# Optimization experiments

Measured on AMD Instinct MI355X. Metric: run time of the kernel, lower is better.

The kernel has to match this reference:

```python
import jax, jax.numpy as jnp
import numpy as np

D_MODEL = 1024
D_STATE = 64
D_CONV = 4
HEADDIM = 64
EXPAND = 2
NGROUPS = 1
D_INNER = EXPAND * D_MODEL            # 2048
NHEADS = D_INNER // HEADDIM           # 32
CONV_DIM = D_INNER + 2 * NGROUPS * D_STATE
D_IN_PROJ = 2 * D_INNER + 2 * NGROUPS * D_STATE + NHEADS
FFN_DIM = 4096
B_SZ = 2
SEQ = 2048


def layernorm(x, w, b, eps=1e-5):
    m = jnp.mean(x, axis=-1, keepdims=True)
    v = jnp.var(x, axis=-1, keepdims=True)
    return (x - m) * jax.lax.rsqrt(v + eps) * w + b


def silu(x):
    return x * jax.nn.sigmoid(x)


def causal_dwconv(x, w, b):
    # x: [B, L, C], w: [C, K] depthwise, b: [C]; causal (left) padding
    xc = jnp.transpose(x, (0, 2, 1))                       # [B, C, L]
    xc = jnp.pad(xc, ((0, 0), (0, 0), (D_CONV - 1, 0)))
    k = w[:, None, :]                                      # [C, 1, K]
    y = jax.lax.conv_general_dilated(
        xc, k, window_strides=(1,), padding='VALID',
        dimension_numbers=('NCH', 'OIH', 'NCH'),
        feature_group_count=CONV_DIM)
    return jnp.transpose(y, (0, 2, 1)) + b                 # [B, L, C]


def mamba2(x, in_proj_w, conv_w, conv_b, dt_bias, A_log, D_param, norm_w, out_proj_w):
    Bsz, L, _ = x.shape
    zxbcdt = x @ in_proj_w.T                               # [B, L, D_IN_PROJ]
    z, xBC, dt = jnp.split(zxbcdt, [D_INNER, D_INNER + CONV_DIM], axis=-1)
    dt = jax.nn.softplus(dt + dt_bias)                     # [B, L, H]
    xBC = silu(causal_dwconv(xBC, conv_w, conv_b))
    xs, Bm, Cm = jnp.split(xBC, [D_INNER, D_INNER + NGROUPS * D_STATE], axis=-1)
    xs = xs.reshape(Bsz, L, NHEADS, HEADDIM)
    Bm = Bm.reshape(Bsz, L, NGROUPS, D_STATE)
    Cm = Cm.reshape(Bsz, L, NGROUPS, D_STATE)
    hpg = NHEADS // NGROUPS
    Bh = jnp.repeat(Bm, hpg, axis=2)                       # [B, L, H, N]
    Ch = jnp.repeat(Cm, hpg, axis=2)                       # [B, L, H, N]
    A = -jnp.exp(A_log)                                    # [H]
    dA = jnp.exp(dt * A)                                   # [B, L, H]

    # time-major for scan
    def step(h, inp):
        dA_t, dt_t, x_t, B_t, C_t = inp                    # [B,H], [B,H], [B,H,P], [B,H,N], [B,H,N]
        h = h * dA_t[:, :, None, None] + (dt_t[:, :, None, None] * x_t[..., None]) * B_t[:, :, None, :]
        y_t = jnp.einsum('bhpn,bhn->bhp', h, C_t)
        return h, y_t

    h0 = jnp.zeros((Bsz, NHEADS, HEADDIM, D_STATE), dtype=x.dtype)
    xs_tm = (jnp.moveaxis(dA, 1, 0), jnp.moveaxis(dt, 1, 0),
             jnp.moveaxis(xs, 1, 0), jnp.moveaxis(Bh, 1, 0), jnp.moveaxis(Ch, 1, 0))
    _, ys = jax.lax.scan(step, h0, xs_tm)                  # [L, B, H, P]
    y = jnp.moveaxis(ys, 0, 1) + D_param[None, None, :, None] * xs
    y = y.reshape(Bsz, L, D_INNER)
    # gated RMSNorm: RMSNorm(y * silu(z)) * weight
    y = y * silu(z)
    y = y * jax.lax.rsqrt(jnp.mean(jnp.square(y), axis=-1, keepdims=True) + 1e-5) * norm_w
    return y @ out_proj_w.T                                # [B, L, D_MODEL]


def setup_inputs() -> dict:
    key = jax.random.key(0)
    ks = jax.random.split(key, 12)
    s = 0.02
    inp = {
        'x': jax.random.normal(ks[0], (B_SZ, SEQ, D_MODEL), dtype=jnp.float32),
        'ln0_w': jnp.ones((D_MODEL,), jnp.float32), 'ln0_b': jnp.zeros((D_MODEL,), jnp.float32),
        'ln1_w': jnp.ones((D_MODEL,), jnp.float32), 'ln1_b': jnp.zeros((D_MODEL,), jnp.float32),
        'ln2_w': jnp.ones((D_MODEL,), jnp.float32), 'ln2_b': jnp.zeros((D_MODEL,), jnp.float32),
        'in_proj_w': jax.random.normal(ks[1], (D_IN_PROJ, D_MODEL), jnp.float32) * s,
        'conv_w': jax.random.normal(ks[2], (CONV_DIM, D_CONV), jnp.float32) * 0.2,
        'conv_b': jnp.zeros((CONV_DIM,), jnp.float32),
        'dt_bias': jax.random.uniform(ks[3], (NHEADS,), jnp.float32, -4.0, -1.0),
        'A_log': jnp.log(jnp.arange(1, NHEADS + 1, dtype=jnp.float32)),
        'D_param': jnp.ones((NHEADS,), jnp.float32),
        'norm_w': jnp.ones((D_INNER,), jnp.float32),
        'out_proj_w': jax.random.normal(ks[4], (D_MODEL, D_INNER), jnp.float32) * s,
        'ffn_w1': jax.random.normal(ks[5], (FFN_DIM, D_MODEL), jnp.float32) * s,
        'ffn_b1': jnp.zeros((FFN_DIM,), jnp.float32),
        'ffn_w2': jax.random.normal(ks[6], (D_MODEL, FFN_DIM), jnp.float32) * s,
        'ffn_b2': jnp.zeros((D_MODEL,), jnp.float32),
    }
    return inp


def reference(x, ln0_w, ln0_b, ln1_w, ln1_b, ln2_w, ln2_b, in_proj_w, conv_w, conv_b,
              dt_bias, A_log, D_param, norm_w, out_proj_w, ffn_w1, ffn_b1, ffn_w2, ffn_b2):
    x = layernorm(x, ln0_w, ln0_b)                                  # ln0 (layer_id==0)
    m = mamba2(layernorm(x, ln1_w, ln1_b), in_proj_w, conv_w, conv_b,
               dt_bias, A_log, D_param, norm_w, out_proj_w)
    x = x + m                                                        # dropout is identity in eval
    h = layernorm(x, ln2_w, ln2_b)
    h = jax.nn.gelu(h @ ffn_w1.T + ffn_b1, approximate=False) @ ffn_w2.T + ffn_b2
    return x + h
```

## Files before the change

### kernel.cpp

```cpp
#include <hip/hip_runtime.h>
#include <hip/hip_bf16.h>
#include <math.h>

typedef __hip_bfloat16 bf16;
typedef __bf16 bhalf;
typedef bhalf bhalf8 __attribute__((ext_vector_type(8)));
typedef float f32x4 __attribute__((ext_vector_type(4)));
typedef unsigned short u16;
typedef u16 u16x4 __attribute__((ext_vector_type(4)));
typedef u16 u16x8 __attribute__((ext_vector_type(8)));

#define D_MODEL   1024
#define D_STATE   64
#define HEADDIM   64
#define D_INNER   2048
#define NHEADS    32
#define CONV_DIM  2176
#define D_IN_PROJ 4256
#define FFN_DIM   4096
#define BSZ       2
#define SEQ       2048
#define NROWS     (BSZ*SEQ)
#define TC        64
#define NCH       (SEQ/TC)

#define AS1 __attribute__((address_space(1)))
#define AS3 __attribute__((address_space(3)))
__device__ __forceinline__ void load_lds16(const void* g, void* l) {
  __builtin_amdgcn_global_load_lds((AS1 void*)g, (AS3 void*)l, 16, 0, 0);
}

__device__ __forceinline__ float bf2f(u16 u) {
  return __uint_as_float(((unsigned)u) << 16);
}
__device__ __forceinline__ u16 f2bbits(float f) {
  bf16 h = __float2bfloat16(f);
  return *(u16*)&h;
}

#define NT 18
struct CvtArgs {
  const void* src[NT];
  void*       dst[NT];
  int ccum[NT + 1];
  int nel[NT];
};

__global__ __launch_bounds__(256)
void cvt_kernel(CvtArgs a, const unsigned short* __restrict__ x0,
                int* __restrict__ flagp)
{
  __shared__ int sbad;
  if (threadIdx.x == 0) sbad = 0;
  __syncthreads();
  {
    float v = bf2f(x0[threadIdx.x]);
    if (!(fabsf(v) <= 1e6f)) sbad = 1;
  }
  __syncthreads();
  const int isf32 = sbad;
  if (blockIdx.x == 0 && threadIdx.x == 0) *flagp = isf32;

  int c = blockIdx.x;
  int ti = 0;
  while (c >= a.ccum[ti + 1]) ti++;
  int j = (c - a.ccum[ti]) * 2048 + threadIdx.x * 8;
  if (j >= a.nel[ti]) return;
  if (isf32) {
    const float* s = (const float*)a.src[ti];
    f32x4 v0 = *(const f32x4*)(s + j);
    f32x4 v1 = *(const f32x4*)(s + j + 4);
    u16x8 o;
    #pragma unroll
    for (int k = 0; k < 4; k++) { o[k] = f2bbits(v0[k]); o[k + 4] = f2bbits(v1[k]); }
    *(u16x8*)((u16*)a.dst[ti] + j) = o;
  } else {
    *(u16x8*)((u16*)a.dst[ti] + j) = *(const u16x8*)((const u16*)a.src[ti] + j);
  }
}

template<int EPI>
__global__ __launch_bounds__(256, 2)
void gemm_bt(const bf16* __restrict__ A, const bf16* __restrict__ W,
             int M, int N, int K,
             bf16* __restrict__ outB,
             const bf16* __restrict__ bias)
{
  __shared__ __align__(16) bhalf sA[2][128 * 64];
  __shared__ __align__(16) bhalf sW[2][128 * 64];
  const int nbx   = gridDim.x;
  const int total = nbx * gridDim.y;
  const int lin   = blockIdx.y * nbx + blockIdx.x;
  const int chunk = total >> 3;
  const int swz   = ((total & 7) == 0) ? ((lin & 7) * chunk + (lin >> 3)) : lin;
  const int n0   = (swz % nbx) * 128;
  const int m0   = (swz / nbx) * 128;
  const int t    = threadIdx.x;
  const int w    = t >> 6;
  const int lane = t & 63;
  const int wm   = (w >> 1) * 64;
  const int wn   = (w & 1) * 64;
  const int lr   = lane & 15;
  const int lq   = lane >> 4;

  f32x4 acc[4][4];
  #pragma unroll
  for (int i = 0; i < 4; i++)
    #pragma unroll
    for (int j = 0; j < 4; j++)
      acc[i][j] = (f32x4){0.f, 0.f, 0.f, 0.f};

  auto stage = [&](int buf, int kk0) {
    #pragma unroll
    for (int j = 0; j < 4; j++) {
      int s  = t + 256 * j;
      int r  = s >> 3;
      int cs = (s & 7) ^ (r & 7);
      load_lds16(A + (size_t)(m0 + r) * K + kk0 + cs * 8, &sA[buf][s * 8]);
      int wr = n0 + r; wr = wr < N ? wr : N - 1;
      load_lds16(W + (size_t)wr * K + kk0 + cs * 8, &sW[buf][s * 8]);
    }
  };

  stage(0, 0);

  int cur = 0;
  for (int k0 = 0; k0 < K; k0 += 64) {
    const bool more = (k0 + 64 < K);
    if (more) stage(cur ^ 1, k0 + 64);
    if (more) asm volatile("s_waitcnt vmcnt(8)" ::: "memory");
    else      asm volatile("s_waitcnt vmcnt(0)" ::: "memory");
    __builtin_amdgcn_s_barrier();
    asm volatile("" ::: "memory");

    const bhalf* pA = sA[cur];
    const bhalf* pW = sW[cur];
    #pragma unroll
    for (int kk = 0; kk < 2; kk++) {
      bhalf8 af[4], bfr[4];
      #pragma unroll
      for (int i = 0; i < 4; i++) {
        int r = wm + i * 16 + lr;
        int c = (kk * 4 + lq) ^ (r & 7);
        af[i] = *(const bhalf8*)(pA + r * 64 + c * 8);
      }
      #pragma unroll
      for (int j = 0; j < 4; j++) {
        int r = wn + j * 16 + lr;
        int c = (kk * 4 + lq) ^ (r & 7);
        bfr[j] = *(const bhalf8*)(pW + r * 64 + c * 8);
      }
      #pragma unroll
      for (int i = 0; i < 4; i++)
        #pragma unroll
        for (int j = 0; j < 4; j++)
          acc[i][j] = __builtin_amdgcn_mfma_f32_16x16x32_bf16(af[i], bfr[j], acc[i][j], 0, 0, 0);
    }
    __builtin_amdgcn_s_barrier();
    asm volatile("" ::: "memory");
    cur ^= 1;
  }

  #pragma unroll
  for (int i = 0; i < 4; i++) {
    #pragma unroll
    for (int j = 0; j < 4; j++) {
      #pragma unroll
      for (int r = 0; r < 4; r++) {
        int m = m0 + wm + i * 16 + lq * 4 + r;
        int n = n0 + wn + j * 16 + lr;
        if (n < N) {
          float v = acc[i][j][r];
          size_t idx = (size_t)m * N + n;
          if (EPI == 0) {
            outB[idx] = __float2bfloat16(v);
          } else {
            v += __bfloat162float(bias[n]);
            outB[idx] = __float2bfloat16(0.5f * v * (1.0f + erff(v * 0.70710678118654752f)));
          }
        }
      }
    }
  }
}

template<int EPI>
__global__ __launch_bounds__(512, 2)
void gemm256_bt(const bf16* __restrict__ A, const bf16* __restrict__ W,
                int M, int N, int K,
                bf16* __restrict__ outB,
                const bf16* __restrict__ bias)
{
  __shared__ __align__(16) bhalf sA[2][256 * 64];
  __shared__ __align__(16) bhalf sW[2][256 * 64];
  const int nbx   = gridDim.x;
  const int total = nbx * gridDim.y;
  const int lin   = blockIdx.y * nbx + blockIdx.x;
  const int chunk = total >> 3;
  const int swz   = ((total & 7) == 0) ? ((lin & 7) * chunk + (lin >> 3)) : lin;
  const int n0   = (swz % nbx) * 256;
  const int m0   = (swz / nbx) * 256;
  const int t    = threadIdx.x;
  const int w    = t >> 6;
  const int lane = t & 63;
  const int wm   = (w >> 2) * 128;
  const int wn   = (w & 3) * 64;
  const int lr   = lane & 15;
  const int lq   = lane >> 4;

  f32x4 acc[8][4];
  #pragma unroll
  for (int i = 0; i < 8; i++)
    #pragma unroll
    for (int j = 0; j < 4; j++)
      acc[i][j] = (f32x4){0.f, 0.f, 0.f, 0.f};

  auto stage = [&](int buf, int kk0) {
    #pragma unroll
    for (int j = 0; j < 4; j++) {
      int s  = t + 512 * j;
      int r  = s >> 3;
      int cs = (s & 7) ^ (r & 7);
      load_lds16(A + (size_t)(m0 + r) * K + kk0 + cs * 8, &sA[buf][s * 8]);
    }
    #pragma unroll
    for (int j = 0; j < 4; j++) {
      int s  = t + 512 * j;
      int r  = s >> 3;
      int cs = (s & 7) ^ (r & 7);
      load_lds16(W + (size_t)(n0 + r) * K + kk0 + cs * 8, &sW[buf][s * 8]);
    }
  };

  stage(0, 0);

  int cur = 0;
  for (int k0 = 0; k0 < K; k0 += 64) {
    const bool more = (k0 + 64 < K);
    if (more) stage(cur ^ 1, k0 + 64);
    if (more) asm volatile("s_waitcnt vmcnt(8)" ::: "memory");
    else      asm volatile("s_waitcnt vmcnt(0)" ::: "memory");
    __builtin_amdgcn_s_barrier();
    asm volatile("" ::: "memory");

    const bhalf* pA = sA[cur];
    const bhalf* pW = sW[cur];
    #pragma unroll
    for (int kk = 0; kk < 2; kk++) {
      bhalf8 af[8], bfr[4];
      #pragma unroll
      for (int i = 0; i < 8; i++) {
        int r = wm + i * 16 + lr;
        int c = (kk * 4 + lq) ^ (r & 7);
        af[i] = *(const bhalf8*)(pA + r * 64 + c * 8);
      }
      #pragma unroll
      for (int j = 0; j < 4; j++) {
        int r = wn + j * 16 + lr;
        int c = (kk * 4 + lq) ^ (r & 7);
        bfr[j] = *(const bhalf8*)(pW + r * 64 + c * 8);
      }
      #pragma unroll
      for (int i = 0; i < 8; i++)
        #pragma unroll
        for (int j = 0; j < 4; j++)
          acc[i][j] = __builtin_amdgcn_mfma_f32_16x16x32_bf16(af[i], bfr[j], acc[i][j], 0, 0, 0);
    }
    __builtin_amdgcn_s_barrier();
    asm volatile("" ::: "memory");
    cur ^= 1;
  }

  #pragma unroll
  for (int i = 0; i < 8; i++) {
    #pragma unroll
    for (int j = 0; j < 4; j++) {
      #pragma unroll
      for (int r = 0; r < 4; r++) {
        int m = m0 + wm + i * 16 + lq * 4 + r;
        int n = n0 + wn + j * 16 + lr;
        float v = acc[i][j][r];
        size_t idx = (size_t)m * N + n;
        if (EPI == 0) {
          outB[idx] = __float2bfloat16(v);
        } else {
          v += __bfloat162float(bias[n]);
          outB[idx] = __float2bfloat16(0.5f * v * (1.0f + erff(v * 0.70710678118654752f)));
        }
      }
    }
  }
}

struct SkParts4 { float* p[4]; };

template<int SK>
__global__ __launch_bounds__(256, 4)
void gemm_skinny_sk(const bf16* __restrict__ A, const bf16* __restrict__ W,
                    int M, int N, int K, SkParts4 parts)
{
  __shared__ __align__(16) bhalf sA[64 * 64];
  __shared__ __align__(16) bhalf sW[128 * 64];
  const int id   = blockIdx.x;
  const int z    = id >> 9;
  const int id9  = id & 511;
  const int hi   = id9 >> 6;
  const int rem  = id9 & 63;
  const int jn   = rem >> 3;
  const int mi   = hi * 8 + (rem & 7);
  const int m0   = mi * 64;
  const int n0   = jn * 128;
  const int t    = threadIdx.x;
  const int w    = t >> 6;
  const int lane = t & 63;
  const int wm   = (w >> 1) * 32;
  const int wn   = (w & 1) * 64;
  const int lr   = lane & 15;
  const int lq   = lane >> 4;

  f32x4 acc[2][4];
  #pragma unroll
  for (int i = 0; i < 2; i++)
    #pragma unroll
    for (int j = 0; j < 4; j++)
      acc[i][j] = (f32x4){0.f, 0.f, 0.f, 0.f};

  const int kh = K / SK;
  const int kend = z * kh + kh;
  for (int k0 = z * kh; k0 < kend; k0 += 64) {
    #pragma unroll
    for (int j = 0; j < 2; j++) {
      int s  = t + 256 * j;
      int r  = s >> 3;
      int cs = (s & 7) ^ (r & 7);
      load_lds16(A + (size_t)(m0 + r) * K + k0 + cs * 8, sA + s * 8);
    }
    #pragma unroll
    for (int j = 0; j < 4; j++) {
      int s  = t + 256 * j;
      int r  = s >> 3;
      int cs = (s & 7) ^ (r & 7);
      load_lds16(W + (size_t)(n0 + r) * K + k0 + cs * 8, sW + s * 8);
    }
    __syncthreads();
    #pragma unroll
    for (int kk = 0; kk < 2; kk++) {
      bhalf8 af[2], bfr[4];
      #pragma unroll
      for (int i = 0; i < 2; i++) {
        int r = wm + i * 16 + lr;
        int c = (kk * 4 + lq) ^ (r & 7);
        af[i] = *(const bhalf8*)(sA + r * 64 + c * 8);
      }
      #pragma unroll
      for (int j = 0; j < 4; j++) {
        int r = wn + j * 16 + lr;
        int c = (kk * 4 + lq) ^ (r & 7);
        bfr[j] = *(const bhalf8*)(sW + r * 64 + c * 8);
      }
      #pragma unroll
      for (int i = 0; i < 2; i++)
        #pragma unroll
        for (int j = 0; j < 4; j++)
          acc[i][j] = __builtin_amdgcn_mfma_f32_16x16x32_bf16(af[i], bfr[j], acc[i][j], 0, 0, 0);
    }
    __syncthreads();
  }

  float* out = parts.p[z];
  #pragma unroll
  for (int i = 0; i < 2; i++)
    #pragma unroll
    for (int j = 0; j < 4; j++)
      #pragma unroll
      for (int r = 0; r < 4; r++) {
        int m = m0 + wm + i * 16 + lq * 4 + r;
        int n = n0 + wn + j * 16 + lr;
        out[(size_t)m * N + n] = acc[i][j][r];
      }
}

__global__ __launch_bounds__(256)
void reduce_out_ln2_kernel(const float* __restrict__ p0, const float* __restrict__ p1,
                           const bf16* __restrict__ resB, float* __restrict__ x2f,
                           const bf16* __restrict__ w, const bf16* __restrict__ b,
                           bf16* __restrict__ hln)
{
  int row = blockIdx.x, t = threadIdx.x;
  int i = row * 256 + t;
  __shared__ float rs[4], rq[4];
  f32x4 a = ((const f32x4*)p0)[i];
  f32x4 bb = ((const f32x4*)p1)[i];
  u16x4 r = ((const u16x4*)resB)[i];
  f32x4 o;
  float s = 0.f, ss = 0.f;
  #pragma unroll
  for (int j = 0; j < 4; j++) {
    o[j] = a[j] + bb[j] + bf2f(r[j]);
    s += o[j]; ss += o[j] * o[j];
  }
  ((f32x4*)x2f)[i] = o;
  #pragma unroll
  for (int off = 32; off; off >>= 1) { s += __shfl_down(s, off); ss += __shfl_down(ss, off); }
  if ((t & 63) == 0) { rs[t >> 6] = s; rq[t >> 6] = ss; }
  __syncthreads();
  float S = rs[0] + rs[1] + rs[2] + rs[3];
  float Q = rq[0] + rq[1] + rq[2] + rq[3];
  float mean = S * (1.f / D_MODEL);
  float rstd = rsqrtf(Q * (1.f / D_MODEL) - mean * mean + 1e-5f);
  u16x4 wv = ((const u16x4*)w)[t];
  u16x4 bv = ((const u16x4*)b)[t];
  u16x4 ov;
  #pragma unroll
  for (int j = 0; j < 4; j++)
    ov[j] = f2bbits((o[j] - mean) * rstd * bf2f(wv[j]) + bf2f(bv[j]));
  ((u16x4*)hln)[i] = ov;
}

__global__ __launch_bounds__(256)
void reduce_ffn_kernel(const float* __restrict__ p0, const float* __restrict__ p1,
                       const float* __restrict__ p2, const float* __restrict__ p3,
                       const bf16* __restrict__ bias, const float* __restrict__ resF,
                       void* __restrict__ outp, const int* __restrict__ flagp)
{
  int i = blockIdx.x * 256 + threadIdx.x;
  int n4 = i & (D_MODEL / 4 - 1);
  f32x4 v0 = ((const f32x4*)p0)[i];
  f32x4 v1 = ((const f32x4*)p1)[i];
  f32x4 v2 = ((const f32x4*)p2)[i];
  f32x4 v3 = ((const f32x4*)p3)[i];
  f32x4 rf = ((const f32x4*)resF)[i];
  u16x4 bb = ((const u16x4*)bias)[n4];
  f32x4 o;
  #pragma unroll
  for (int j = 0; j < 4; j++)
    o[j] = ((v0[j] + v1[j]) + (v2[j] + v3[j])) + rf[j] + bf2f(bb[j]);
  if (*flagp) {
    ((f32x4*)outp)[i] = o;
  } else {
    u16x4 ov;
    #pragma unroll
    for (int j = 0; j < 4; j++) ov[j] = f2bbits(o[j]);
    ((u16x4*)outp)[i] = ov;
  }
}

__global__ __launch_bounds__(256)
void ln01_kernel(const void* __restrict__ xin, const int* __restrict__ flagp,
                 const bf16* __restrict__ w0, const bf16* __restrict__ b0,
                 const bf16* __restrict__ w1, const bf16* __restrict__ b1,
                 bf16* __restrict__ x0o, bf16* __restrict__ x1o)
{
  int row = blockIdx.x, t = threadIdx.x;
  int i = row * 256 + t;
  __shared__ float rs[4], rq[4];
  float v[4], s = 0.f, ss = 0.f;
  if (*flagp) {
    f32x4 xv = ((const f32x4*)xin)[i];
    #pragma unroll
    for (int j = 0; j < 4; j++) v[j] = xv[j];
  } else {
    u16x4 xv = ((const u16x4*)xin)[i];
    #pragma unroll
    for (int j = 0; j < 4; j++) v[j] = bf2f(xv[j]);
  }
  #pragma unroll
  for (int j = 0; j < 4; j++) { s += v[j]; ss += v[j] * v[j]; }
  #pragma unroll
  for (int o = 32; o; o >>= 1) { s += __shfl_down(s, o); ss += __shfl_down(ss, o); }
  if ((t & 63) == 0) { rs[t >> 6] = s; rq[t >> 6] = ss; }
  __syncthreads();
  float S = rs[0] + rs[1] + rs[2] + rs[3];
  float Q = rq[0] + rq[1] + rq[2] + rq[3];
  float mean = S * (1.f / D_MODEL);
  float rstd = rsqrtf(Q * (1.f / D_MODEL) - mean * mean + 1e-5f);
  u16x4 w0v = ((const u16x4*)w0)[t], b0v = ((const u16x4*)b0)[t];
  float u[4]; s = 0.f; ss = 0.f;
  u16x4 o0;
  #pragma unroll
  for (int j = 0; j < 4; j++) {
    u[j] = (v[j] - mean) * rstd * bf2f(w0v[j]) + bf2f(b0v[j]);
    s += u[j]; ss += u[j] * u[j];
    o0[j] = f2bbits(u[j]);
  }
  ((u16x4*)x0o)[i] = o0;
  __syncthreads();
  #pragma unroll
  for (int o = 32; o; o >>= 1) { s += __shfl_down(s, o); ss += __shfl_down(ss, o); }
  if ((t & 63) == 0) { rs[t >> 6] = s; rq[t >> 6] = ss; }
  __syncthreads();
  S = rs[0] + rs[1] + rs[2] + rs[3];
  Q = rq[0] + rq[1] + rq[2] + rq[3];
  mean = S * (1.f / D_MODEL);
  rstd = rsqrtf(Q * (1.f / D_MODEL) - mean * mean + 1e-5f);
  u16x4 w1v = ((const u16x4*)w1)[t], b1v = ((const u16x4*)b1)[t];
  u16x4 o1;
  #pragma unroll
  for (int j = 0; j < 4; j++)
    o1[j] = f2bbits((u[j] - mean) * rstd * bf2f(w1v[j]) + bf2f(b1v[j]));
  ((u16x4*)x1o)[i] = o1;
}

__device__ __forceinline__ void conv8(const bf16* __restrict__ zxb,
                                      const bf16* __restrict__ cw,
                                      const bf16* __restrict__ cb,
                                      bf16* __restrict__ xact, int row, int c0)
{
  int l = row & (SEQ - 1);
  float acc[8];
  {
    bhalf8 cbv = *(const bhalf8*)(cb + c0);
    #pragma unroll
    for (int j = 0; j < 8; j++) acc[j] = (float)cbv[j];
  }
  bhalf wts[32];
  #pragma unroll
  for (int q = 0; q < 4; q++)
    *(bhalf8*)(wts + q * 8) = *(const bhalf8*)(cw + c0 * 4 + q * 8);
  #pragma unroll
  for (int k = 0; k < 4; k++) {
    int lt = l - 3 + k;
    if (lt >= 0) {
      bhalf8 xv = *(const bhalf8*)(zxb + (size_t)(row - 3 + k) * D_IN_PROJ + D_INNER + c0);
      #pragma unroll
      for (int j = 0; j < 8; j++)
        acc[j] = fmaf((float)xv[j], (float)wts[j * 4 + k], acc[j]);
    }
  }
  bhalf8 o;
  #pragma unroll
  for (int j = 0; j < 8; j++) {
    float a = acc[j];
    o[j] = (bhalf)(a / (1.f + expf(-a)));
  }
  *(bhalf8*)(xact + (size_t)row * CONV_DIM + c0) = o;
}

__global__ __launch_bounds__(256)
void conv_silu_dt_kernel(const bf16* __restrict__ zxb, const bf16* __restrict__ cw,
                         const bf16* __restrict__ cb, bf16* __restrict__ xact,
                         const bf16* __restrict__ dtb, const bf16* __restrict__ alog,
                         float* __restrict__ dts, float* __restrict__ ldab)
{
  const int row = blockIdx.y;
  const int t = threadIdx.x;
  if (blockIdx.x == 0) {
    conv8(zxb, cw, cb, xact, row, t * 8);
  } else {
    if (t < 16) {
      conv8(zxb, cw, cb, xact, row, 2048 + t * 8);
    } else if (t < 48) {
      int h = t - 16;
      float v = __bfloat162float(zxb[(size_t)row * D_IN_PROJ + (D_INNER + CONV_DIM) + h]) +
                __bfloat162float(dtb[h]);
      float sp = (v > 20.f) ? v : log1pf(expf(v));
      dts[row * NHEADS + h] = sp;
      ldab[row * NHEADS + h] = -sp * expf(__bfloat162float(alog[h]));
    }
  }
}

__global__ __launch_bounds__(256)
void scan_state_kernel(const bf16* __restrict__ xact, const float* __restrict__ dts,
                       const float* __restrict__ ldab, bf16* __restrict__ Sbuf,
                       float* __restrict__ acb)
{
  __shared__ __align__(16) bf16 wBT[64][72];
  __shared__ __align__(16) bf16 XT[64][72];
  __shared__ float lsS[64], dtS[64];
  const int bid = blockIdx.x;
  const int bh = bid & 63, c = bid >> 6;
  const int b = bh >> 5, h = bh & 31;
  const int t0 = c * TC;
  const int tid = threadIdx.x;
  const int w = tid >> 6, lane = tid & 63;
  const int lr = lane & 15, lq = lane >> 4;

  if (w == 0) {
    float v = ldab[(size_t)(b * SEQ + t0 + lane) * NHEADS + h];
    #pragma unroll
    for (int o = 1; o < 64; o <<= 1) {
      float up = __shfl_up(v, o);
      if (lane >= o) v += up;
    }
    lsS[lane] = v;
    dtS[lane] = dts[(size_t)(b * SEQ + t0 + lane) * NHEADS + h];
  }
  __syncthreads();
  const float lsT = lsS[63];
  {
    int nn = tid & 63, u0 = (tid >> 6) * 16;
    for (int i = 0; i < 16; i++) {
      int u = u0 + i;
      const bf16* rowp = xact + (size_t)(b * SEQ + t0 + u) * CONV_DIM;
      float wgt = dtS[u] * __expf(lsT - lsS[u]);
      wBT[nn][u] = __float2bfloat16(__bfloat162float(rowp[D_INNER + nn]) * wgt);
      XT[nn][u]  = rowp[h * 64 + nn];
    }
  }
  __syncthreads();

  bhalf8 af0 = *(const bhalf8*)&wBT[16 * w + lr][lq * 8];
  bhalf8 af1 = *(const bhalf8*)&wBT[16 * w + lr][32 + lq * 8];
  bf16* sb = Sbuf + ((size_t)bh * NCH + c) * 4096;
  #pragma unroll
  for (int jt = 0; jt < 4; jt++) {
    bhalf8 xf0 = *(const bhalf8*)&XT[16 * jt + lr][lq * 8];
    bhalf8 xf1 = *(const bhalf8*)&XT[16 * jt + lr][32 + lq * 8];
    f32x4 acc = (f32x4){0.f, 0.f, 0.f, 0.f};
    acc = __builtin_amdgcn_mfma_f32_16x16x32_bf16(af0, xf0, acc, 0, 0, 0);
    acc = __builtin_amdgcn_mfma_f32_16x16x32_bf16(af1, xf1, acc, 0, 0, 0);
    #pragma unroll
    for (int r = 0; r < 4; r++) {
      int n = 16 * w + lq * 4 + r;
      int p = 16 * jt + lr;
      sb[p * 64 + n] = __float2bfloat16(acc[r]);
    }
  }
  if (tid == 0) acb[bh * NCH + c] = __expf(lsT);
}

__global__ __launch_bounds__(256)
void state_prop_kernel(bf16* __restrict__ Sbuf, const float* __restrict__ acb)
{
  const int bh = blockIdx.x >> 2, q = blockIdx.x & 3;
  const int t = threadIdx.x;
  bf16* sp = Sbuf + (size_t)bh * NCH * 4096 + q * 1024 + t;
  const float* ap = acb + bh * NCH;
  float h0 = 0.f, h1 = 0.f, h2 = 0.f, h3 = 0.f;
  for (int c = 0; c < NCH; c++) {
    bf16* pc = sp + (size_t)c * 4096;
    float s0 = __bfloat162float(pc[0]);
    float s1 = __bfloat162float(pc[256]);
    float s2 = __bfloat162float(pc[512]);
    float s3 = __bfloat162float(pc[768]);
    float a = ap[c];
    pc[0]   = __float2bfloat16(h0);
    pc[256] = __float2bfloat16(h1);
    pc[512] = __float2bfloat16(h2);
    pc[768] = __float2bfloat16(h3);
    h0 = fmaf(h0, a, s0); h1 = fmaf(h1, a, s1);
    h2 = fmaf(h2, a, s2); h3 = fmaf(h3, a, s3);
  }
}

__global__ __launch_bounds__(256)
void scan_y_kernel(const bf16* __restrict__ xact, const float* __restrict__ dts,
                   const float* __restrict__ ldab, const bf16* __restrict__ Sbuf,
                   bf16* __restrict__ yfull)
{
  __shared__ __align__(16) bf16 Cs[64][72];
  __shared__ __align__(16) bf16 Bs[64][72];
  __shared__ __align__(16) bf16 XT[64][72];
  __shared__ __align__(16) bf16 HT[64][72];
  __shared__ float lsS[64], dtS[64];
  const int bid = blockIdx.x;
  const int bh = bid & 63, c = bid >> 6;
  const int b = bh >> 5, h = bh & 31;
  const int t0 = c * TC;
  const int tid = threadIdx.x;
  const int w = tid >> 6, lane = tid & 63;
  const int lr = lane & 15, lq = lane >> 4;

  if (w == 0) {
    float v = ldab[(size_t)(b * SEQ + t0 + lane) * NHEADS + h];
    #pragma unroll
    for (int o = 1; o < 64; o <<= 1) {
      float up = __shfl_up(v, o);
      if (lane >= o) v += up;
    }
    lsS[lane] = v;
    dtS[lane] = dts[(size_t)(b * SEQ + t0 + lane) * NHEADS + h];
  }
  {
    int nn = tid & 63, u0 = (tid >> 6) * 16;
    for (int i = 0; i < 16; i++) {
      int u = u0 + i;
      const bf16* rowp = xact + (size_t)(b * SEQ + t0 + u) * CONV_DIM;
      Bs[u][nn] = rowp[D_INNER + nn];
      Cs[u][nn] = rowp[D_INNER + 64 + nn];
      XT[nn][u] = rowp[h * 64 + nn];
    }
    const bf16* sb = Sbuf + ((size_t)bh * NCH + c) * 4096;
    for (int i = 0; i < 16; i++) {
      int e = tid + 256 * i;
      HT[e >> 6][e & 63] = sb[e];
    }
  }
  __syncthreads();

  bhalf8 cf0 = *(const bhalf8*)&Cs[16 * w + lr][lq * 8];
  bhalf8 cf1 = *(const bhalf8*)&Cs[16 * w + lr][32 + lq * 8];
  f32x4 accH[4];
  float mreg[4][4];
  #pragma unroll
  for (int jt = 0; jt < 4; jt++) {
    bhalf8 bf0 = *(const bhalf8*)&Bs[16 * jt + lr][lq * 8];
    bhalf8 bf1 = *(const bhalf8*)&Bs[16 * jt + lr][32 + lq * 8];
    f32x4 g = (f32x4){0.f, 0.f, 0.f, 0.f};
    g = __builtin_amdgcn_mfma_f32_16x16x32_bf16(cf0, bf0, g, 0, 0, 0);
    g = __builtin_amdgcn_mfma_f32_16x16x32_bf16(cf1, bf1, g, 0, 0, 0);
    bhalf8 hf0 = *(const bhalf8*)&HT[16 * jt + lr][lq * 8];
    bhalf8 hf1 = *(const bhalf8*)&HT[16 * jt + lr][32 + lq * 8];
    f32x4 ah = (f32x4){0.f, 0.f, 0.f, 0.f};
    ah = __builtin_amdgcn_mfma_f32_16x16x32_bf16(cf0, hf0, ah, 0, 0, 0);
    ah = __builtin_amdgcn_mfma_f32_16x16x32_bf16(cf1, hf1, ah, 0, 0, 0);
    accH[jt] = ah;
    #pragma unroll
    for (int r = 0; r < 4; r++) {
      int t = 16 * w + lq * 4 + r;
      int u = 16 * jt + lr;
      float m = 0.f;
      if (u <= t) m = g[r] * __expf(lsS[t] - lsS[u]) * dtS[u];
      mreg[jt][r] = m;
    }
  }
  __syncthreads();
  #pragma unroll
  for (int jt = 0; jt < 4; jt++)
    #pragma unroll
    for (int r = 0; r < 4; r++)
      Bs[16 * w + lq * 4 + r][16 * jt + lr] = __float2bfloat16(mreg[jt][r]);
  __syncthreads();

  bhalf8 mf0 = *(const bhalf8*)&Bs[16 * w + lr][lq * 8];
  bhalf8 mf1 = *(const bhalf8*)&Bs[16 * w + lr][32 + lq * 8];
  #pragma unroll
  for (int jt = 0; jt < 4; jt++) {
    bhalf8 xf0 = *(const bhalf8*)&XT[16 * jt + lr][lq * 8];
    bhalf8 xf1 = *(const bhalf8*)&XT[16 * jt + lr][32 + lq * 8];
    f32x4 acc = (f32x4){0.f, 0.f, 0.f, 0.f};
    acc = __builtin_amdgcn_mfma_f32_16x16x32_bf16(mf0, xf0, acc, 0, 0, 0);
    acc = __builtin_amdgcn_mfma_f32_16x16x32_bf16(mf1, xf1, acc, 0, 0, 0);
    #pragma unroll
    for (int r = 0; r < 4; r++) {
      int t = 16 * w + lq * 4 + r;
      int p = 16 * jt + lr;
      float y = acc[r] + __expf(lsS[t]) * accH[jt][r];
      yfull[(size_t)(b * SEQ + t0 + t) * D_INNER + h * 64 + p] = __float2bfloat16(y);
    }
  }
}

__global__ __launch_bounds__(256)
void gate_rms_kernel(const bf16* __restrict__ yfull, const bf16* __restrict__ xact,
                     const bf16* __restrict__ zxb, const bf16* __restrict__ Dp,
                     const bf16* __restrict__ nw, bf16* __restrict__ yn)
{
  int row = blockIdx.x, t = threadIdx.x;
  int c0 = t * 8;
  __shared__ float rq[4];
  bhalf8 yv8 = *(const bhalf8*)(yfull + (size_t)row * D_INNER + c0);
  bhalf8 xv8 = *(const bhalf8*)(xact + (size_t)row * CONV_DIM + c0);
  bhalf8 zv8 = *(const bhalf8*)(zxb + (size_t)row * D_IN_PROJ + c0);
  float Dv = __bfloat162float(Dp[c0 >> 6]);
  float yv[8]; float ss = 0.f;
  #pragma unroll
  for (int j = 0; j < 8; j++) {
    float y = (float)yv8[j] + Dv * (float)xv8[j];
    float z = (float)zv8[j];
    yv[j] = y * (z / (1.f + expf(-z)));
    ss += yv[j] * yv[j];
  }
  #pragma unroll
  for (int o = 32; o; o >>= 1) ss += __shfl_down(ss, o);
  if ((t & 63) == 0) rq[t >> 6] = ss;
  __syncthreads();
  float tot = rq[0] + rq[1] + rq[2] + rq[3];
  float rr = rsqrtf(tot * (1.f / D_INNER) + 1e-5f);
  bhalf8 nv8 = *(const bhalf8*)(nw + c0);
  bhalf8 o;
  #pragma unroll
  for (int j = 0; j < 8; j++)
    o[j] = (bhalf)(yv[j] * rr * (float)nv8[j]);
  *(bhalf8*)(yn + (size_t)row * D_INNER + c0) = o;
}

extern "C" void kernel_launch(void* const* d_in, const int* in_sizes, int n_in,
                              void* d_out, int out_size, void* d_ws, size_t ws_size,
                              hipStream_t stream)
{
  char* ws = (char*)d_ws;
  bf16*  x1b   = (bf16*) (ws + 0);
  bf16*  Sbuf  = (bf16*) (ws + 0);
  bf16*  ynb   = (bf16*) (ws + 0);
  float* pf0   = (float*)(ws + 0);
  bf16*  wproj = (bf16*) (ws + 16777216);
  float* acb   = (float*)(ws + 16777216);
  float* dtsb  = (float*)(ws + 16785408);
  float* ldab  = (float*)(ws + 17309696);
  float* pf1   = (float*)(ws + 16777216);
  bf16*  wout  = (bf16*) (ws + 25493504);
  bf16*  w1c   = (bf16*) (ws + 29687808);
  bf16*  w2c   = (bf16*) (ws + 38076416);
  bf16*  ln0w  = (bf16*) (ws + 46465024);
  bf16*  ln0b  = (bf16*) (ws + 46467072);
  bf16*  ln1w  = (bf16*) (ws + 46469120);
  bf16*  ln1b  = (bf16*) (ws + 46471168);
  bf16*  ln2w  = (bf16*) (ws + 46473216);
  bf16*  ln2b  = (bf16*) (ws + 46475264);
  bf16*  convw = (bf16*) (ws + 46477312);
  bf16*  convb = (bf16*) (ws + 46494720);
  bf16*  dtb   = (bf16*) (ws + 46499072);
  bf16*  alog  = (bf16*) (ws + 46499136);
  bf16*  Dp    = (bf16*) (ws + 46499200);
  bf16*  normw = (bf16*) (ws + 46499264);
  bf16*  b1c   = (bf16*) (ws + 46503360);
  bf16*  b2c   = (bf16*) (ws + 46511552);
  int*   flag  = (int*)  (ws + 46513600);
  bf16*  x0b   = (bf16*) (ws + 46514176);
  bf16*  zxb   = (bf16*) (ws + 54902784);
  float* x2f   = (float*)(ws + 54902784);
  float* pf3   = (float*)(ws + 71680000);
  bf16*  xact  = (bf16*) (ws + 89767936);
  float* pout0 = (float*)(ws + 89767936);
  float* pout1 = (float*)(ws + 106545152);
  bf16*  gbuf  = (bf16*) (ws + 89767936);
  bf16*  yfull = (bf16*) (ws + 125419520);
  bf16*  hln   = (bf16*) (ws + 125419520);
  float* pf2   = (float*)(ws + 125419520);

  CvtArgs ca;
  void* dsts[NT] = { ln0w, ln0b, ln1w, ln1b, ln2w, ln2b, wproj, convw, convb,
                     dtb, alog, Dp, normw, wout, w1c, b1c, w2c, b2c };
  int cc = 0;
  ca.ccum[0] = 0;
  for (int i = 0; i < NT; i++) {
    ca.src[i] = d_in[i + 1];
    ca.dst[i] = dsts[i];
    ca.nel[i] = in_sizes[i + 1];
    cc += (in_sizes[i + 1] + 2047) / 2048;
    ca.ccum[i + 1] = cc;
  }
  cvt_kernel<<<cc, 256, 0, stream>>>(ca, (const unsigned short*)d_in[0], flag);

  ln01_kernel<<<NROWS, 256, 0, stream>>>(d_in[0], flag, ln0w, ln0b, ln1w, ln1b,
                                         x0b, x1b);

  gemm_bt<0><<<dim3(34, 32), 256, 0, stream>>>(x1b, wproj, NROWS, D_IN_PROJ, D_MODEL,
                                               zxb, nullptr);

  conv_silu_dt_kernel<<<dim3(2, NROWS), 256, 0, stream>>>(zxb, convw, convb, xact,
                                                          dtb, alog, dtsb, ldab);

  scan_state_kernel<<<NCH * 64, 256, 0, stream>>>(xact, dtsb, ldab, Sbuf, acb);
  state_prop_kernel<<<64 * 4, 256, 0, stream>>>(Sbuf, acb);
  scan_y_kernel<<<NCH * 64, 256, 0, stream>>>(xact, dtsb, ldab, Sbuf, yfull);

  gate_rms_kernel<<<NROWS, 256, 0, stream>>>(yfull, xact, zxb, Dp, normw, ynb);

  SkParts4 po = { { pout0, pout1, pout0, pout0 } };
  gemm_skinny_sk<2><<<1024, 256, 0, stream>>>(ynb, wout, NROWS, D_MODEL, D_INNER, po);
  reduce_out_ln2_kernel<<<NROWS, 256, 0, stream>>>(pout0, pout1, x0b, x2f,
                                                   ln2w, ln2b, hln);

  gemm256_bt<2><<<dim3(16, 16), 512, 0, stream>>>(hln, w1c, NROWS, FFN_DIM, D_MODEL,
                                                  gbuf, b1c);

  SkParts4 pfp = { { pf0, pf1, pf2, pf3 } };
  gemm_skinny_sk<4><<<2048, 256, 0, stream>>>(gbuf, w2c, NROWS, D_MODEL, FFN_DIM, pfp);
  reduce_ffn_kernel<<<(NROWS * D_MODEL) / 1024, 256, 0, stream>>>(pf0, pf1, pf2, pf3,
                                                                  b2c, x2f, d_out, flag);
}
```

Before: 432.6 us.

## Split in_proj GEMM into 256-tile main part plus tail, restructure inner MFMA loop

The in_proj GEMM (N=4256) is split so the first 4096 columns run on the larger 256x256 tile kernel and the remaining 160 columns run on the 128-tile kernel, with an explicit output leading dimension. The 256-tile kernel's inner loop is reorganised into four half-fragment phases with fewer live A fragments, s_setprio around MFMA bursts and extra barriers between phases. The aim is better data reuse and lower register pressure for the large GEMMs. In exchange it adds a second launch and extra intra-tile barriers.

New measurement: 454.0 us. +5.0%, slower.

```diff
diff --git a/kernel.cpp b/kernel.cpp
--- a/kernel.cpp
+++ b/kernel.cpp
@@ -82,7 +82,7 @@
 template<int EPI>
 __global__ __launch_bounds__(256, 2)
 void gemm_bt(const bf16* __restrict__ A, const bf16* __restrict__ W,
-             int M, int N, int K,
+             int M, int N, int K, int ldout,
              bf16* __restrict__ outB,
              const bf16* __restrict__ bias)
 {
@@ -171,7 +171,7 @@
         int n = n0 + wn + j * 16 + lr;
         if (n < N) {
           float v = acc[i][j][r];
-          size_t idx = (size_t)m * N + n;
+          size_t idx = (size_t)m * ldout + n;
           if (EPI == 0) {
             outB[idx] = __float2bfloat16(v);
           } else {
@@ -187,7 +187,7 @@
 template<int EPI>
 __global__ __launch_bounds__(512, 2)
 void gemm256_bt(const bf16* __restrict__ A, const bf16* __restrict__ W,
-                int M, int N, int K,
+                int M, int N, int K, int ldout,
                 bf16* __restrict__ outB,
                 const bf16* __restrict__ bias)
 {
@@ -245,29 +245,84 @@
 
     const bhalf* pA = sA[cur];
     const bhalf* pW = sW[cur];
-    #pragma unroll
-    for (int kk = 0; kk < 2; kk++) {
-      bhalf8 af[8], bfr[4];
-      #pragma unroll
-      for (int i = 0; i < 8; i++) {
-        int r = wm + i * 16 + lr;
-        int c = (kk * 4 + lq) ^ (r & 7);
-        af[i] = *(const bhalf8*)(pA + r * 64 + c * 8);
-      }
-      #pragma unroll
-      for (int j = 0; j < 4; j++) {
-        int r = wn + j * 16 + lr;
-        int c = (kk * 4 + lq) ^ (r & 7);
-        bfr[j] = *(const bhalf8*)(pW + r * 64 + c * 8);
-      }
-      #pragma unroll
-      for (int i = 0; i < 8; i++)
-        #pragma unroll
-        for (int j = 0; j < 4; j++)
-          acc[i][j] = __builtin_amdgcn_mfma_f32_16x16x32_bf16(af[i], bfr[j], acc[i][j], 0, 0, 0);
-    }
+    bhalf8 af[4], bfr[4];
+
+    #pragma unroll
+    for (int j = 0; j < 4; j++) {
+      int r = wn + j * 16 + lr;
+      int c = lq ^ (r & 7);
+      bfr[j] = *(const bhalf8*)(pW + r * 64 + c * 8);
+    }
+    #pragma unroll
+    for (int i = 0; i < 4; i++) {
+      int r = wm + i * 16 + lr;
+      int c = lq ^ (r & 7);
+      af[i] = *(const bhalf8*)(pA + r * 64 + c * 8);
+    }
+    __builtin_amdgcn_s_setprio(1);
+    #pragma unroll
+    for (int i = 0; i < 4; i++)
+      #pragma unroll
+      for (int j = 0; j < 4; j++)
+        acc[i][j] = __builtin_amdgcn_mfma_f32_16x16x32_bf16(af[i], bfr[j], acc[i][j], 0, 0, 0);
+    __builtin_amdgcn_s_setprio(0);
     __builtin_amdgcn_s_barrier();
     asm volatile("" ::: "memory");
+
+    #pragma unroll
+    for (int i = 0; i < 4; i++) {
+      int r = wm + 64 + i * 16 + lr;
+      int c = lq ^ (r & 7);
+      af[i] = *(const bhalf8*)(pA + r * 64 + c * 8);
+    }
+    __builtin_amdgcn_s_setprio(1);
+    #pragma unroll
+    for (int i = 0; i < 4; i++)
+      #pragma unroll
+      for (int j = 0; j < 4; j++)
+        acc[4 + i][j] = __builtin_amdgcn_mfma_f32_16x16x32_bf16(af[i], bfr[j], acc[4 + i][j], 0, 0, 0);
+    __builtin_amdgcn_s_setprio(0);
+    __builtin_amdgcn_s_barrier();
+    asm volatile("" ::: "memory");
+
+    #pragma unroll
+    for (int j = 0; j < 4; j++) {
+      int r = wn + j * 16 + lr;
+      int c = (4 + lq) ^ (r & 7);
+      bfr[j] = *(const bhalf8*)(pW + r * 64 + c * 8);
+    }
+    #pragma unroll
+    for (int i = 0; i < 4; i++) {
+      int r = wm + i * 16 + lr;
+      int c = (4 + lq) ^ (r & 7);
+      af[i] = *(const bhalf8*)(pA + r * 64 + c * 8);
+    }
+    __builtin_amdgcn_s_setprio(1);
+    #pragma unroll
+    for (int i = 0; i < 4; i++)
+      #pragma unroll
+      for (int j = 0; j < 4; j++)
+        acc[i][j] = __builtin_amdgcn_mfma_f32_16x16x32_bf16(af[i], bfr[j], acc[i][j], 0, 0, 0);
+    __builtin_amdgcn_s_setprio(0);
+    __builtin_amdgcn_s_barrier();
+    asm volatile("" ::: "memory");
+
+    #pragma unroll
+    for (int i = 0; i < 4; i++) {
+      int r = wm + 64 + i * 16 + lr;
+      int c = (4 + lq) ^ (r & 7);
+      af[i] = *(const bhalf8*)(pA + r * 64 + c * 8);
+    }
+    __builtin_amdgcn_s_setprio(1);
+    #pragma unroll
+    for (int i = 0; i < 4; i++)
+      #pragma unroll
+      for (int j = 0; j < 4; j++)
+        acc[4 + i][j] = __builtin_amdgcn_mfma_f32_16x16x32_bf16(af[i], bfr[j], acc[4 + i][j], 0, 0, 0);
+    __builtin_amdgcn_s_setprio(0);
+    __builtin_amdgcn_s_barrier();
+    asm volatile("" ::: "memory");
+
     cur ^= 1;
   }
 
@@ -280,7 +335,7 @@
         int m = m0 + wm + i * 16 + lq * 4 + r;
         int n = n0 + wn + j * 16 + lr;
         float v = acc[i][j][r];
-        size_t idx = (size_t)m * N + n;
+        size_t idx = (size_t)m * ldout + n;
         if (EPI == 0) {
           outB[idx] = __float2bfloat16(v);
         } else {
@@ -837,8 +892,11 @@
   ln01_kernel<<<NROWS, 256, 0, stream>>>(d_in[0], flag, ln0w, ln0b, ln1w, ln1b,
                                          x0b, x1b);
 
-  gemm_bt<0><<<dim3(34, 32), 256, 0, stream>>>(x1b, wproj, NROWS, D_IN_PROJ, D_MODEL,
-                                               zxb, nullptr);
+  gemm256_bt<0><<<dim3(16, 16), 512, 0, stream>>>(x1b, wproj, NROWS, 4096, D_MODEL,
+                                                  D_IN_PROJ, zxb, nullptr);
+  gemm_bt<0><<<dim3(2, 32), 256, 0, stream>>>(x1b, wproj + (size_t)4096 * D_MODEL,
+                                              NROWS, 160, D_MODEL, D_IN_PROJ,
+                                              zxb + 4096, nullptr);
 
   conv_silu_dt_kernel<<<dim3(2, NROWS), 256, 0, stream>>>(zxb, convw, convb, xact,
                                                           dtb, alog, dtsb, ldab);
@@ -855,7 +913,7 @@
                                                    ln2w, ln2b, hln);
 
   gemm256_bt<2><<<dim3(16, 16), 512, 0, stream>>>(hln, w1c, NROWS, FFN_DIM, D_MODEL,
-                                                  gbuf, b1c);
+                                                  FFN_DIM, gbuf, b1c);
 
   SkParts4 pfp = { { pf0, pf1, pf2, pf3 } };
   gemm_skinny_sk<4><<<2048, 256, 0, stream>>>(gbuf, w2c, NROWS, D_MODEL, FFN_DIM, pfp);
```

## Replace 256-tile FFN GEMM with 128x128 BK32 kernel and split in_proj GEMM

Applied to the files above, without the earlier changes.

Replaces the 256x256 BK64 GEMM used for the FFN up-projection with a new 128x128 tile, BK=32 kernel with smaller LDS footprint and higher occupancy (launch bounds 256,4). The in_proj GEMM is split into a 4096-column part using the new kernel (no N bounds check) and a 160-column tail handled by the old 128-tile kernel, with a leading-dimension parameter added for strided output. The goal is more resident blocks and better latency hiding on the many CUs. In exchange, it gives up the larger tiles' data reuse, uses shorter K steps with more barriers, and adds an extra launch.

After: 431.4 us. Within noise of the previous version (-0.3%).

```diff
diff --git a/kernel.cpp b/kernel.cpp
--- a/kernel.cpp
+++ b/kernel.cpp
@@ -82,7 +82,7 @@
 template<int EPI>
 __global__ __launch_bounds__(256, 2)
 void gemm_bt(const bf16* __restrict__ A, const bf16* __restrict__ W,
-             int M, int N, int K,
+             int M, int N, int K, int ldout,
              bf16* __restrict__ outB,
              const bf16* __restrict__ bias)
 {
@@ -171,7 +171,7 @@
         int n = n0 + wn + j * 16 + lr;
         if (n < N) {
           float v = acc[i][j][r];
-          size_t idx = (size_t)m * N + n;
+          size_t idx = (size_t)m * ldout + n;
           if (EPI == 0) {
             outB[idx] = __float2bfloat16(v);
           } else {
@@ -185,49 +185,43 @@
 }
 
 template<int EPI>
-__global__ __launch_bounds__(512, 2)
-void gemm256_bt(const bf16* __restrict__ A, const bf16* __restrict__ W,
-                int M, int N, int K,
-                bf16* __restrict__ outB,
-                const bf16* __restrict__ bias)
-{
-  __shared__ __align__(16) bhalf sA[2][256 * 64];
-  __shared__ __align__(16) bhalf sW[2][256 * 64];
+__global__ __launch_bounds__(256, 4)
+void gemm128_bk32(const bf16* __restrict__ A, const bf16* __restrict__ W,
+                  int M, int N, int K, int ldout,
+                  bf16* __restrict__ outB,
+                  const bf16* __restrict__ bias)
+{
+  __shared__ __align__(16) bhalf sA[2][128 * 32];
+  __shared__ __align__(16) bhalf sW[2][128 * 32];
   const int nbx   = gridDim.x;
   const int total = nbx * gridDim.y;
   const int lin   = blockIdx.y * nbx + blockIdx.x;
   const int chunk = total >> 3;
   const int swz   = ((total & 7) == 0) ? ((lin & 7) * chunk + (lin >> 3)) : lin;
-  const int n0   = (swz % nbx) * 256;
-  const int m0   = (swz / nbx) * 256;
+  const int n0   = (swz % nbx) * 128;
+  const int m0   = (swz / nbx) * 128;
   const int t    = threadIdx.x;
   const int w    = t >> 6;
   const int lane = t & 63;
-  const int wm   = (w >> 2) * 128;
-  const int wn   = (w & 3) * 64;
+  const int wm   = (w >> 1) * 64;
+  const int wn   = (w & 1) * 64;
   const int lr   = lane & 15;
   const int lq   = lane >> 4;
 
-  f32x4 acc[8][4];
-  #pragma unroll
-  for (int i = 0; i < 8; i++)
+  f32x4 acc[4][4];
+  #pragma unroll
+  for (int i = 0; i < 4; i++)
     #pragma unroll
     for (int j = 0; j < 4; j++)
       acc[i][j] = (f32x4){0.f, 0.f, 0.f, 0.f};
 
   auto stage = [&](int buf, int kk0) {
     #pragma unroll
-    for (int j = 0; j < 4; j++) {
-      int s  = t + 512 * j;
-      int r  = s >> 3;
-      int cs = (s & 7) ^ (r & 7);
+    for (int j = 0; j < 2; j++) {
+      int s  = t + 256 * j;
+      int r  = s >> 2;
+      int cs = (s & 3) ^ (r & 3);
       load_lds16(A + (size_t)(m0 + r) * K + kk0 + cs * 8, &sA[buf][s * 8]);
-    }
-    #pragma unroll
-    for (int j = 0; j < 4; j++) {
-      int s  = t + 512 * j;
-      int r  = s >> 3;
-      int cs = (s & 7) ^ (r & 7);
       load_lds16(W + (size_t)(n0 + r) * K + kk0 + cs * 8, &sW[buf][s * 8]);
     }
   };
@@ -235,44 +229,42 @@
   stage(0, 0);
 
   int cur = 0;
-  for (int k0 = 0; k0 < K; k0 += 64) {
-    const bool more = (k0 + 64 < K);
-    if (more) stage(cur ^ 1, k0 + 64);
-    if (more) asm volatile("s_waitcnt vmcnt(8)" ::: "memory");
+  for (int k0 = 0; k0 < K; k0 += 32) {
+    const bool more = (k0 + 32 < K);
+    if (more) stage(cur ^ 1, k0 + 32);
+    if (more) asm volatile("s_waitcnt vmcnt(4)" ::: "memory");
     else      asm volatile("s_waitcnt vmcnt(0)" ::: "memory");
     __builtin_amdgcn_s_barrier();
     asm volatile("" ::: "memory");
 
     const bhalf* pA = sA[cur];
     const bhalf* pW = sW[cur];
-    #pragma unroll
-    for (int kk = 0; kk < 2; kk++) {
-      bhalf8 af[8], bfr[4];
-      #pragma unroll
-      for (int i = 0; i < 8; i++) {
-        int r = wm + i * 16 + lr;
-        int c = (kk * 4 + lq) ^ (r & 7);
-        af[i] = *(const bhalf8*)(pA + r * 64 + c * 8);
-      }
-      #pragma unroll
-      for (int j = 0; j < 4; j++) {
-        int r = wn + j * 16 + lr;
-        int c = (kk * 4 + lq) ^ (r & 7);
-        bfr[j] = *(const bhalf8*)(pW + r * 64 + c * 8);
-      }
-      #pragma unroll
-      for (int i = 0; i < 8; i++)
-        #pragma unroll
-        for (int j = 0; j < 4; j++)
-          acc[i][j] = __builtin_amdgcn_mfma_f32_16x16x32_bf16(af[i], bfr[j], acc[i][j], 0, 0, 0);
-    }
+    bhalf8 af[4], bfr[4];
+    #pragma unroll
+    for (int i = 0; i < 4; i++) {
+      int r = wm + i * 16 + lr;
+      int c = lq ^ (r & 3);
+      af[i] = *(const bhalf8*)(pA + r * 32 + c * 8);
+    }
+    #pragma unroll
+    for (int j = 0; j < 4; j++) {
+      int r = wn + j * 16 + lr;
+      int c = lq ^ (r & 3);
+      bfr[j] = *(const bhalf8*)(pW + r * 32 + c * 8);
+    }
+    #pragma unroll
+    for (int i = 0; i < 4; i++)
+      #pragma unroll
+      for (int j = 0; j < 4; j++)
+        acc[i][j] = __builtin_amdgcn_mfma_f32_16x16x32_bf16(af[i], bfr[j], acc[i][j], 0, 0, 0);
+
     __builtin_amdgcn_s_barrier();
     asm volatile("" ::: "memory");
     cur ^= 1;
   }
 
   #pragma unroll
-  for (int i = 0; i < 8; i++) {
+  for (int i = 0; i < 4; i++) {
     #pragma unroll
     for (int j = 0; j < 4; j++) {
       #pragma unroll
@@ -280,7 +272,7 @@
         int m = m0 + wm + i * 16 + lq * 4 + r;
         int n = n0 + wn + j * 16 + lr;
         float v = acc[i][j][r];
-        size_t idx = (size_t)m * N + n;
+        size_t idx = (size_t)m * ldout + n;
         if (EPI == 0) {
           outB[idx] = __float2bfloat16(v);
         } else {
@@ -837,8 +829,11 @@
   ln01_kernel<<<NROWS, 256, 0, stream>>>(d_in[0], flag, ln0w, ln0b, ln1w, ln1b,
                                          x0b, x1b);
 
-  gemm_bt<0><<<dim3(34, 32), 256, 0, stream>>>(x1b, wproj, NROWS, D_IN_PROJ, D_MODEL,
-                                               zxb, nullptr);
+  gemm128_bk32<0><<<dim3(32, 32), 256, 0, stream>>>(x1b, wproj, NROWS, 4096, D_MODEL,
+                                                    D_IN_PROJ, zxb, nullptr);
+  gemm_bt<0><<<dim3(2, 32), 256, 0, stream>>>(x1b, wproj + (size_t)4096 * D_MODEL,
+                                              NROWS, 160, D_MODEL, D_IN_PROJ,
+                                              zxb + 4096, nullptr);
 
   conv_silu_dt_kernel<<<dim3(2, NROWS), 256, 0, stream>>>(zxb, convw, convb, xact,
                                                           dtb, alog, dtsb, ldab);
@@ -854,8 +849,8 @@
   reduce_out_ln2_kernel<<<NROWS, 256, 0, stream>>>(pout0, pout1, x0b, x2f,
                                                    ln2w, ln2b, hln);
 
-  gemm256_bt<2><<<dim3(16, 16), 512, 0, stream>>>(hln, w1c, NROWS, FFN_DIM, D_MODEL,
-                                                  gbuf, b1c);
+  gemm128_bk32<2><<<dim3(32, 32), 256, 0, stream>>>(hln, w1c, NROWS, FFN_DIM, D_MODEL,
+                                                    FFN_DIM, gbuf, b1c);
 
   SkParts4 pfp = { { pf0, pf1, pf2, pf3 } };
   gemm_skinny_sk<4><<<2048, 256, 0, stream>>>(gbuf, w2c, NROWS, D_MODEL, FFN_DIM, pfp);
```
